# Performance work log

Measured on AMD Instinct MI355X. Metric: run time of the kernel, lower is better.

## Reference

```python
import jax, jax.numpy as jnp
import numpy as np


def setup_inputs() -> dict:
    key = jax.random.key(0)
    k1, k2, k3 = jax.random.split(key, 3)
    B, N, C, H, W = 4, 6, 80, 16, 44
    image_features = jax.random.normal(k1, (B * N, C, H, W), dtype=jnp.float32)
    # eye + small perturbation keeps the 3x3 intrinsics block invertible
    intrinsics = jnp.eye(4, dtype=jnp.float32) + 0.1 * jax.random.normal(k2, (B, N, 4, 4), dtype=jnp.float32)
    extrinsics = jnp.eye(4, dtype=jnp.float32) + 0.1 * jax.random.normal(k3, (B, N, 4, 4), dtype=jnp.float32)
    return {"image_features": image_features, "intrinsics": intrinsics,
            "extrinsics": extrinsics, "depth_bins": 59}


def reference(image_features, intrinsics, extrinsics, depth_bins):
    BN, C, H, W = image_features.shape
    N = intrinsics.shape[1]
    B = BN // N
    dt = image_features.dtype
    depths = jnp.linspace(0.1, 1.0, depth_bins).astype(dt)  # (D,)
    feats = image_features.reshape(B, N, C, H, W)

    # pixel homogeneous coords, matching torch meshgrid(indexing='ij') + flatten
    yy, xx = jnp.meshgrid(jnp.arange(H), jnp.arange(W), indexing='ij')
    xy1 = jnp.stack([xx.ravel(), yy.ravel(), jnp.ones(H * W)], axis=0).astype(dt)  # (3, HW)

    K_inv = jnp.linalg.inv(intrinsics[:, :, :3, :3])            # (B,N,3,3)
    rays = jnp.einsum('bnij,jp->bnip', K_inv, xy1)              # (B,N,3,HW)

    # softmax over spatial dim (dim=3 of (B,N,C,HW) in the torch code)
    depth_probs = jax.nn.softmax(feats.reshape(B, N, C, H * W), axis=3)

    # In the original, only the LAST 4 channels of the (4C+1)-channel homogeneous
    # volume enter the extrinsic matmul: the [x,y,z] coords of channel C-1 plus 1.
    d_last = depth_probs[:, :, -1]                              # (B,N,HW)
    # (B,N,3,HW,D) = rays * (prob * depth)
    pts = rays[..., None] * (d_last[:, :, None, :, None] * depths)

    R = extrinsics[:, :, :3, :3]                                # (B,N,3,3)
    t = extrinsics[:, :, :3, 3]                                 # (B,N,3)
    world = jnp.einsum('bnij,bnjpd->bnipd', R, pts) + t[:, :, :, None, None]
    world = world.reshape(B, N, 3, H, W, depth_bins)

    feats_rep = jnp.broadcast_to(feats[..., None], (B, N, C, H, W, depth_bins))
    return jnp.concatenate([world, feats_rep], axis=2)         # (B,N,3+C,H,W,D)
```

## Files before the change

kernel.cpp:

```cpp
#include <hip/hip_runtime.h>


#define BB 4
#define NN 6
#define CC 80
#define HH 16
#define WW 44
#define DD 59
#define BN (BB*NN)
#define PP (HH*WW)
#define CHO (CC+3)
#define WD (WW*DD)
#define NQ4 (WD/4)
#define HLOC HH
#define DSTEP (0.9f/58.f)

typedef float fx4 __attribute__((ext_vector_type(4)));

__device__ inline float waveMax(float v) {
#pragma unroll
    for (int o = 32; o; o >>= 1) v = fmaxf(v, __shfl_xor(v, o));
    return v;
}
__device__ inline float waveSum(float v) {
#pragma unroll
    for (int o = 32; o; o >>= 1) v += __shfl_xor(v, o);
    return v;
}

__global__ __launch_bounds__(256) void lss_all(const float* __restrict__ feats,
                                               const float* __restrict__ intr,
                                               const float* __restrict__ extr,
                                               float* __restrict__ out) {
    const int blk  = blockIdx.x;
    const int ch   = blk % CHO;
    const int bn   = blk / CHO;
    const int tid  = threadIdx.x;
    const bool world = (ch < 3);

    __shared__ float sf[PP];
    __shared__ float valw[HLOC][WW + 1];
    __shared__ float sred[4];
    __shared__ float sbc[2];

    float tval = 0.f;

    if (world) {
        const float* f = feats + ((size_t)bn * CC + (CC - 1)) * PP;
        float m = -1e30f;
        for (int p = tid; p < PP; p += 256) { float v = f[p]; sf[p] = v; m = fmaxf(m, v); }
        m = waveMax(m);
        if ((tid & 63) == 0) sred[tid >> 6] = m;
        __syncthreads();
        if (tid == 0) sbc[0] = fmaxf(fmaxf(sred[0], sred[1]), fmaxf(sred[2], sred[3]));
        __syncthreads();
        const float mm = sbc[0];
        float s = 0.f;
        for (int p = tid; p < PP; p += 256) { float e = expf(sf[p] - mm); sf[p] = e; s += e; }
        s = waveSum(s);
        if ((tid & 63) == 0) sred[tid >> 6] = s;
        __syncthreads();
        if (tid == 0) sbc[1] = sred[0] + sred[1] + sred[2] + sred[3];
        __syncthreads();
        const float inv = 1.0f / sbc[1];

        const float* K = intr + bn * 16;
        float a = K[0], b = K[1], c = K[2];
        float d = K[4], e = K[5], ff = K[6];
        float g = K[8], h9 = K[9], i9 = K[10];
        float det = a * (e * i9 - ff * h9) - b * (d * i9 - ff * g) + c * (d * h9 - e * g);
        float id = 1.0f / det;
        float kinv[9] = {
            (e * i9 - ff * h9) * id, (c * h9 - b * i9) * id, (b * ff - c * e) * id,
            (ff * g - d * i9) * id,  (a * i9 - c * g) * id,  (c * d - a * ff) * id,
            (d * h9 - e * g) * id,   (b * g - a * h9) * id,  (a * e - b * d) * id
        };
        const float* E = extr + bn * 16;
        float M0 = E[ch * 4 + 0] * kinv[0] + E[ch * 4 + 1] * kinv[3] + E[ch * 4 + 2] * kinv[6];
        float M1 = E[ch * 4 + 0] * kinv[1] + E[ch * 4 + 1] * kinv[4] + E[ch * 4 + 2] * kinv[7];
        float M2 = E[ch * 4 + 0] * kinv[2] + E[ch * 4 + 1] * kinv[5] + E[ch * 4 + 2] * kinv[8];
        tval = E[ch * 4 + 3];

        for (int t2 = tid; t2 < PP; t2 += 256) {
            int hl = t2 / WW;
            int w  = t2 - hl * WW;
            float ray = M0 * (float)w + M1 * (float)hl + M2;
            valw[hl][w] = ray * sf[t2] * inv;
        }
    } else {
        const float* frow = feats + ((size_t)bn * CC + (ch - 3)) * PP;
        for (int t2 = tid; t2 < PP; t2 += 256) {
            int hl = t2 / WW;
            int w  = t2 - hl * WW;
            valw[hl][w] = frow[t2];
        }
    }
    if (tid < HLOC) valw[tid][WW] = 0.f;
    __syncthreads();

    int   wA[3];
    int   cross[3][4];
    float sc[3][4];
#pragma unroll
    for (int i = 0; i < 3; ++i) {
        int q = tid + 256 * i;
        if (q < NQ4) {
            int base = 4 * q;
            int w    = base / DD;
            int dlo  = base - DD * w;
            wA[i] = w;
#pragma unroll
            for (int k = 0; k < 4; ++k) {
                int dd   = dlo + k;
                int cr   = (dd >= DD) ? 1 : 0;
                int deff = dd - cr * DD;
                cross[i][k] = cr;
                sc[i][k] = 0.1f + (float)deff * DSTEP;
            }
        }
    }

    float* obase = out + ((size_t)(bn * CHO + ch)) * HH * WD;

    if (world) {
        for (int hl = 0; hl < HLOC; ++hl) {
            const float* vr = valw[hl];
            float* orow = obase + (size_t)hl * WD;
#pragma unroll
            for (int i = 0; i < 3; ++i) {
                int q = tid + 256 * i;
                if (q < NQ4) {
                    float v0 = vr[wA[i]];
                    float v1 = vr[wA[i] + 1];
                    fx4 r;
                    r.x = (cross[i][0] ? v1 : v0) * sc[i][0] + tval;
                    r.y = (cross[i][1] ? v1 : v0) * sc[i][1] + tval;
                    r.z = (cross[i][2] ? v1 : v0) * sc[i][2] + tval;
                    r.w = (cross[i][3] ? v1 : v0) * sc[i][3] + tval;
                    *(fx4*)(orow + 4 * q) = r;
                }
            }
        }
    } else {
        for (int hl = 0; hl < HLOC; ++hl) {
            const float* vr = valw[hl];
            float* orow = obase + (size_t)hl * WD;
#pragma unroll
            for (int i = 0; i < 3; ++i) {
                int q = tid + 256 * i;
                if (q < NQ4) {
                    float v0 = vr[wA[i]];
                    float v1 = vr[wA[i] + 1];
                    fx4 r;
                    r.x = cross[i][0] ? v1 : v0;
                    r.y = cross[i][1] ? v1 : v0;
                    r.z = cross[i][2] ? v1 : v0;
                    r.w = cross[i][3] ? v1 : v0;
                    *(fx4*)(orow + 4 * q) = r;
                }
            }
        }
    }
}

extern "C" void kernel_launch(void* const* d_in, const int* in_sizes, int n_in,
                              void* d_out, int out_size, void* d_ws, size_t ws_size,
                              hipStream_t stream) {
    const float* feats = (const float*)d_in[0];
    const float* intr  = (const float*)d_in[1];
    const float* extr  = (const float*)d_in[2];
    float* out = (float*)d_out;

    lss_all<<<BN * CHO, 256, 0, stream>>>(feats, intr, extr, out);
}
```

Baseline: 70.20 us.

## Split into softmax prep kernel and grid-stride flat output sweep

Moves the softmax, intrinsics inverse and ray projection into a small prep kernel that writes per-(bn,channel) world values and translations to workspace. A second kernel then sweeps the whole output as a flat float4 index space with a fixed 2048-block grid-stride loop, decoding coordinates by integer division. This removes the redundant per-block softmax and the uneven work of the world-channel blocks. In exchange it adds a second launch, a workspace round trip, and per-element index division in a write-bound kernel.

```diff
diff --git a/kernel.cpp b/kernel.cpp
--- a/kernel.cpp
+++ b/kernel.cpp
@@ -11,11 +11,12 @@
 #define PP (HH*WW)
 #define CHO (CC+3)
 #define WD (WW*DD)
-#define NQ4 (WD/4)
-#define HLOC HH
 #define DSTEP (0.9f/58.f)
+#define NF4 20684928u
+#define SWEEPB 2048
 
 typedef float fx4 __attribute__((ext_vector_type(4)));
+typedef unsigned int uint;
 
 __device__ inline float waveMax(float v) {
 #pragma unroll
@@ -28,138 +29,103 @@
     return v;
 }
 
-__global__ __launch_bounds__(256) void lss_all(const float* __restrict__ feats,
-                                               const float* __restrict__ intr,
-                                               const float* __restrict__ extr,
-                                               float* __restrict__ out) {
-    const int blk  = blockIdx.x;
-    const int ch   = blk % CHO;
-    const int bn   = blk / CHO;
-    const int tid  = threadIdx.x;
-    const bool world = (ch < 3);
-
+__global__ __launch_bounds__(256) void lss_prep(const float* __restrict__ feats,
+                                                const float* __restrict__ intr,
+                                                const float* __restrict__ extr,
+                                                float* __restrict__ Vw,
+                                                float* __restrict__ Tarr) {
+    const int bn = blockIdx.x;
+    const int tid = threadIdx.x;
     __shared__ float sf[PP];
-    __shared__ float valw[HLOC][WW + 1];
     __shared__ float sred[4];
     __shared__ float sbc[2];
 
-    float tval = 0.f;
+    const float* f = feats + ((size_t)bn * CC + (CC - 1)) * PP;
+    float m = -1e30f;
+    for (int p = tid; p < PP; p += 256) { float v = f[p]; sf[p] = v; m = fmaxf(m, v); }
+    m = waveMax(m);
+    if ((tid & 63) == 0) sred[tid >> 6] = m;
+    __syncthreads();
+    if (tid == 0) sbc[0] = fmaxf(fmaxf(sred[0], sred[1]), fmaxf(sred[2], sred[3]));
+    __syncthreads();
+    const float mm = sbc[0];
+    float s = 0.f;
+    for (int p = tid; p < PP; p += 256) { float e = expf(sf[p] - mm); sf[p] = e; s += e; }
+    s = waveSum(s);
+    if ((tid & 63) == 0) sred[tid >> 6] = s;
+    __syncthreads();
+    if (tid == 0) sbc[1] = sred[0] + sred[1] + sred[2] + sred[3];
+    __syncthreads();
+    const float inv = 1.0f / sbc[1];
 
-    if (world) {
-        const float* f = feats + ((size_t)bn * CC + (CC - 1)) * PP;
-        float m = -1e30f;
-        for (int p = tid; p < PP; p += 256) { float v = f[p]; sf[p] = v; m = fmaxf(m, v); }
-        m = waveMax(m);
-        if ((tid & 63) == 0) sred[tid >> 6] = m;
-        __syncthreads();
-        if (tid == 0) sbc[0] = fmaxf(fmaxf(sred[0], sred[1]), fmaxf(sred[2], sred[3]));
-        __syncthreads();
-        const float mm = sbc[0];
-        float s = 0.f;
-        for (int p = tid; p < PP; p += 256) { float e = expf(sf[p] - mm); sf[p] = e; s += e; }
-        s = waveSum(s);
-        if ((tid & 63) == 0) sred[tid >> 6] = s;
-        __syncthreads();
-        if (tid == 0) sbc[1] = sred[0] + sred[1] + sred[2] + sred[3];
-        __syncthreads();
-        const float inv = 1.0f / sbc[1];
-
-        const float* K = intr + bn * 16;
-        float a = K[0], b = K[1], c = K[2];
-        float d = K[4], e = K[5], ff = K[6];
-        float g = K[8], h9 = K[9], i9 = K[10];
-        float det = a * (e * i9 - ff * h9) - b * (d * i9 - ff * g) + c * (d * h9 - e * g);
-        float id = 1.0f / det;
-        float kinv[9] = {
-            (e * i9 - ff * h9) * id, (c * h9 - b * i9) * id, (b * ff - c * e) * id,
-            (ff * g - d * i9) * id,  (a * i9 - c * g) * id,  (c * d - a * ff) * id,
-            (d * h9 - e * g) * id,   (b * g - a * h9) * id,  (a * e - b * d) * id
-        };
-        const float* E = extr + bn * 16;
+    const float* K = intr + bn * 16;
+    float a = K[0], b = K[1], c = K[2];
+    float d = K[4], e = K[5], ff = K[6];
+    float g = K[8], h9 = K[9], i9 = K[10];
+    float det = a * (e * i9 - ff * h9) - b * (d * i9 - ff * g) + c * (d * h9 - e * g);
+    float id = 1.0f / det;
+    float kinv[9] = {
+        (e * i9 - ff * h9) * id, (c * h9 - b * i9) * id, (b * ff - c * e) * id,
+        (ff * g - d * i9) * id,  (a * i9 - c * g) * id,  (c * d - a * ff) * id,
+        (d * h9 - e * g) * id,   (b * g - a * h9) * id,  (a * e - b * d) * id
+    };
+    const float* E = extr + bn * 16;
+#pragma unroll
+    for (int ch = 0; ch < 3; ++ch) {
         float M0 = E[ch * 4 + 0] * kinv[0] + E[ch * 4 + 1] * kinv[3] + E[ch * 4 + 2] * kinv[6];
         float M1 = E[ch * 4 + 0] * kinv[1] + E[ch * 4 + 1] * kinv[4] + E[ch * 4 + 2] * kinv[7];
         float M2 = E[ch * 4 + 0] * kinv[2] + E[ch * 4 + 1] * kinv[5] + E[ch * 4 + 2] * kinv[8];
-        tval = E[ch * 4 + 3];
+        float* vrow = Vw + (size_t)(bn * 3 + ch) * PP;
+        for (int p = tid; p < PP; p += 256) {
+            int hl = p / WW;
+            int w  = p - hl * WW;
+            float ray = M0 * (float)w + M1 * (float)hl + M2;
+            vrow[p] = ray * sf[p] * inv;
+        }
+        if (tid == 0) Tarr[bn * 3 + ch] = E[ch * 4 + 3];
+    }
+}
 
-        for (int t2 = tid; t2 < PP; t2 += 256) {
-            int hl = t2 / WW;
-            int w  = t2 - hl * WW;
-            float ray = M0 * (float)w + M1 * (float)hl + M2;
-            valw[hl][w] = ray * sf[t2] * inv;
-        }
-    } else {
-        const float* frow = feats + ((size_t)bn * CC + (ch - 3)) * PP;
-        for (int t2 = tid; t2 < PP; t2 += 256) {
-            int hl = t2 / WW;
-            int w  = t2 - hl * WW;
-            valw[hl][w] = frow[t2];
-        }
-    }
-    if (tid < HLOC) valw[tid][WW] = 0.f;
-    __syncthreads();
+__global__ __launch_bounds__(256) void lss_sweep(const float* __restrict__ feats,
+                                                 const float* __restrict__ Vw,
+                                                 const float* __restrict__ Tarr,
+                                                 float* __restrict__ out) {
+    const uint stride = gridDim.x * 256u;
+    for (uint fq = blockIdx.x * 256u + threadIdx.x; fq < NF4; fq += stride) {
+        uint r  = fq / 649u;
+        uint q  = fq - 649u * r;
+        uint c  = q << 2;
+        uint w  = c / 59u;
+        uint d  = c - 59u * w;
+        uint s  = r >> 4;
+        uint hl = r & 15u;
+        uint bn = s / 83u;
+        uint ch = s - 83u * bn;
+        uint cw = (d >= 56u) ? 1u : 0u;
+        uint kc = 59u - d;
 
-    int   wA[3];
-    int   cross[3][4];
-    float sc[3][4];
-#pragma unroll
-    for (int i = 0; i < 3; ++i) {
-        int q = tid + 256 * i;
-        if (q < NQ4) {
-            int base = 4 * q;
-            int w    = base / DD;
-            int dlo  = base - DD * w;
-            wA[i] = w;
+        fx4 v;
+        if (ch < 3u) {
+            uint wrow = s - 80u * bn;
+            uint widx = wrow * (uint)PP + hl * 44u + w;
+            float T  = Tarr[wrow];
+            float vA = Vw[widx];
+            float vB = Vw[widx + cw];
 #pragma unroll
             for (int k = 0; k < 4; ++k) {
-                int dd   = dlo + k;
-                int cr   = (dd >= DD) ? 1 : 0;
-                int deff = dd - cr * DD;
-                cross[i][k] = cr;
-                sc[i][k] = 0.1f + (float)deff * DSTEP;
+                bool crossed = ((uint)k >= kc);
+                float val = crossed ? vB : vA;
+                uint dk = d + (uint)k - (crossed ? 59u : 0u);
+                v[k] = val * (0.1f + (float)dk * DSTEP) + T;
             }
+        } else {
+            uint fi = (s - 3u * bn - 3u) * (uint)PP + hl * 44u + w;
+            float vA = feats[fi];
+            float vB = feats[fi + cw];
+#pragma unroll
+            for (int k = 0; k < 4; ++k) v[k] = ((uint)k >= kc) ? vB : vA;
         }
-    }
-
-    float* obase = out + ((size_t)(bn * CHO + ch)) * HH * WD;
-
-    if (world) {
-        for (int hl = 0; hl < HLOC; ++hl) {
-            const float* vr = valw[hl];
-            float* orow = obase + (size_t)hl * WD;
-#pragma unroll
-            for (int i = 0; i < 3; ++i) {
-                int q = tid + 256 * i;
-                if (q < NQ4) {
-                    float v0 = vr[wA[i]];
-                    float v1 = vr[wA[i] + 1];
-                    fx4 r;
-                    r.x = (cross[i][0] ? v1 : v0) * sc[i][0] + tval;
-                    r.y = (cross[i][1] ? v1 : v0) * sc[i][1] + tval;
-                    r.z = (cross[i][2] ? v1 : v0) * sc[i][2] + tval;
-                    r.w = (cross[i][3] ? v1 : v0) * sc[i][3] + tval;
-                    *(fx4*)(orow + 4 * q) = r;
-                }
-            }
-        }
-    } else {
-        for (int hl = 0; hl < HLOC; ++hl) {
-            const float* vr = valw[hl];
-            float* orow = obase + (size_t)hl * WD;
-#pragma unroll
-            for (int i = 0; i < 3; ++i) {
-                int q = tid + 256 * i;
-                if (q < NQ4) {
-                    float v0 = vr[wA[i]];
-                    float v1 = vr[wA[i] + 1];
-                    fx4 r;
-                    r.x = cross[i][0] ? v1 : v0;
-                    r.y = cross[i][1] ? v1 : v0;
-                    r.z = cross[i][2] ? v1 : v0;
-                    r.w = cross[i][3] ? v1 : v0;
-                    *(fx4*)(orow + 4 * q) = r;
-                }
-            }
-        }
+        ((fx4*)out)[fq] = v;
     }
 }
 
@@ -169,7 +135,10 @@
     const float* feats = (const float*)d_in[0];
     const float* intr  = (const float*)d_in[1];
     const float* extr  = (const float*)d_in[2];
-    float* out = (float*)d_out;
+    float* out  = (float*)d_out;
+    float* Vw   = (float*)d_ws;
+    float* Tarr = (float*)d_ws + 50688 + 16;
 
-    lss_all<<<BN * CHO, 256, 0, stream>>>(feats, intr, extr, out);
+    lss_prep<<<BN, 256, 0, stream>>>(feats, intr, extr, Vw, Tarr);
+    lss_sweep<<<SWEEPB, 256, 0, stream>>>(feats, Vw, Tarr, out);
 }
```

Result: faster. 67.69 us (-3.6%).
